# Kernel tuning notes

Hardware: AMD Instinct MI355X
Metric: run time of the kernel (lower is better)

## Reference

```python
import jax, jax.numpy as jnp
import numpy as np

D_MODEL = 1024
NUM_HEADS = 16
D_K = D_MODEL // NUM_HEADS
BATCH = 4
SEQ = 2048


def setup_inputs() -> dict:
    key = jax.random.key(0)
    ks = jax.random.split(key, 12)
    s = 0.02
    inp = {
        "Q": jax.random.normal(ks[0], (BATCH, SEQ, D_MODEL), jnp.float32),
        "K": jax.random.normal(ks[1], (BATCH, SEQ, D_MODEL), jnp.float32),
        "V": jax.random.normal(ks[2], (BATCH, SEQ, D_MODEL), jnp.float32),
        "mask": jnp.tril(jnp.ones((SEQ, SEQ), jnp.int32)),  # causal: 0 = masked
        "Wq": jax.random.normal(ks[3], (D_MODEL, D_MODEL), jnp.float32) * s,
        "bq": jax.random.normal(ks[4], (D_MODEL,), jnp.float32) * s,
        "Wk": jax.random.normal(ks[5], (D_MODEL, D_MODEL), jnp.float32) * s,
        "bk": jax.random.normal(ks[6], (D_MODEL,), jnp.float32) * s,
        "Wv": jax.random.normal(ks[7], (D_MODEL, D_MODEL), jnp.float32) * s,
        "bv": jax.random.normal(ks[8], (D_MODEL,), jnp.float32) * s,
        "Wo": jax.random.normal(ks[9], (D_MODEL, D_MODEL), jnp.float32) * s,
        "bo": jax.random.normal(ks[10], (D_MODEL,), jnp.float32) * s,
    }
    return inp


def _split_heads(x):
    # (b, s, d_model) -> (b, h, s, d_k)
    b, s, _ = x.shape
    return x.reshape(b, s, NUM_HEADS, D_K).transpose(0, 2, 1, 3)


def reference(Q, K, V, mask, Wq, bq, Wk, bk, Wv, bv, Wo, bo):
    # Linear projections (torch Linear: x @ W^T + b)
    q = _split_heads(Q @ Wq.T + bq)  # (b, h, s, dk)
    k = _split_heads(K @ Wk.T + bk)
    v = _split_heads(V @ Wv.T + bv)
    scale = 1.0 / jnp.sqrt(jnp.asarray(D_K, q.dtype))
    scores = jnp.einsum("bhqd,bhkd->bhqk", q, k) * scale  # (b, h, s, s)
    scores = jnp.where(mask == 0, jnp.asarray(-jnp.inf, scores.dtype), scores)
    attn = jax.nn.softmax(scores, axis=-1)
    out = jnp.einsum("bhqk,bhkd->bhqd", attn, v)  # (b, h, s, dk)
    b, h, s, dk = out.shape
    out = out.transpose(0, 2, 1, 3).reshape(b, s, h * dk)  # combine heads
    return out @ Wo.T + bo
```

## Files before the change

### kernel.cpp

```cpp
#include <hip/hip_runtime.h>


typedef _Float16 f16;
typedef _Float16 f16x8 __attribute__((ext_vector_type(8)));
typedef _Float16 f16x4 __attribute__((ext_vector_type(4)));
typedef float floatx4 __attribute__((ext_vector_type(4)));

#define SEQ 2048
#define DM 1024
#define NH 16
#define DK 64
#define MR 8192

__device__ __forceinline__ void gl_lds16(const void* g, void* lds) {
    __builtin_amdgcn_global_load_lds(
        (const __attribute__((address_space(1))) unsigned int*)g,
        (__attribute__((address_space(3))) unsigned int*)lds,
        16, 0, 0);
}

struct ConvArgs {
    const float* s[7];
    f16* d[7];
};

__global__ __launch_bounds__(256) void convk(ConvArgs a) {
    int bx = blockIdx.x;
    int t, base;
    if (bx < 3 * 8192) { t = bx / 8192; base = bx - t * 8192; }
    else { int r = bx - 3 * 8192; t = 3 + r / 1024; base = r - (t - 3) * 1024; }
    int i = base * 256 + threadIdx.x;
    float4 v = ((const float4*)a.s[t])[i];
    f16x4 o;
    o.x = (f16)v.x; o.y = (f16)v.y; o.z = (f16)v.z; o.w = (f16)v.w;
    ((f16x4*)a.d[t])[i] = o;
}

template <int MODE>
__device__ __forceinline__ void gemm_body(
    const f16* __restrict__ A, const f16* __restrict__ W,
    const float* __restrict__ bias, void* __restrict__ outp,
    int m0, int n0, f16* As, f16* Bs)
{
    const int tid = threadIdx.x;
    const int wave = tid >> 6, lane = tid & 63;
    const int quad = lane >> 4, ln = lane & 15;
    const int wr = wave >> 1, wc = wave & 1;

    floatx4 acc[4][4] = {};

    for (int kt = 0; kt < 16; ++kt) {
        const int k0 = kt * 64;
#pragma unroll
        for (int s = 0; s < 4; ++s) {
            int c = s * 256 + tid;
            int row = c >> 3, lc = (c & 7) ^ (row & 7);
            gl_lds16(A + (size_t)(m0 + row) * 1024 + k0 + lc * 8,
                     (char*)As + (s * 256 + wave * 64) * 16);
        }
#pragma unroll
        for (int s = 0; s < 4; ++s) {
            int c = s * 256 + tid;
            int row = c >> 3, lc = (c & 7) ^ (row & 7);
            gl_lds16(W + (size_t)(n0 + row) * 1024 + k0 + lc * 8,
                     (char*)Bs + (s * 256 + wave * 64) * 16);
        }
        __syncthreads();
#pragma unroll
        for (int kk = 0; kk < 64; kk += 32) {
            const int cb = kk >> 3;
            f16x8 af[4], bf[4];
#pragma unroll
            for (int i = 0; i < 4; ++i) {
                int row = wr * 64 + i * 16 + ln;
                af[i] = *(const f16x8*)&As[row * 64 + (((cb + quad) ^ (ln & 7)) << 3)];
            }
#pragma unroll
            for (int j = 0; j < 4; ++j) {
                int row = wc * 64 + j * 16 + ln;
                bf[j] = *(const f16x8*)&Bs[row * 64 + (((cb + quad) ^ (ln & 7)) << 3)];
            }
#pragma unroll
            for (int i = 0; i < 4; ++i)
#pragma unroll
                for (int j = 0; j < 4; ++j)
                    acc[i][j] = __builtin_amdgcn_mfma_f32_16x16x32_f16(
                        af[i], bf[j], acc[i][j], 0, 0, 0);
        }
        __syncthreads();
    }

#pragma unroll
    for (int i = 0; i < 4; ++i) {
#pragma unroll
        for (int j = 0; j < 4; ++j) {
            int col = n0 + wc * 64 + j * 16 + ln;
            float bc = bias[col];
            int rowb = m0 + wr * 64 + i * 16 + quad * 4;
#pragma unroll
            for (int r = 0; r < 4; ++r) {
                float v = acc[i][j][r] + bc;
                int rm = rowb + r;
                if (MODE == 2) {
                    ((float*)outp)[(size_t)rm * 1024 + col] = v;
                } else {
                    int bb = rm >> 11, ss = rm & 2047;
                    int hh = col >> 6, dd = col & 63;
                    f16* o = (f16*)outp;
                    if (MODE == 0)
                        o[(((size_t)(bb * 16 + hh)) * 2048 + ss) * 64 + dd] = (f16)v;
                    else
                        o[(((size_t)(bb * 16 + hh)) * 64 + dd) * 2048 + ss] = (f16)v;
                }
            }
        }
    }
}

struct G3Args {
    const f16* A[3]; const f16* W[3]; const float* b[3]; f16* o[3];
};

__global__ __launch_bounds__(256, 2) void gemm_qkv(G3Args g) {
    __shared__ alignas(16) f16 As[128 * 64];
    __shared__ alignas(16) f16 Bs[128 * 64];
    const int z = blockIdx.z;
    const int m0 = blockIdx.x * 128, n0 = blockIdx.y * 128;
    if (z < 2)
        gemm_body<0>(g.A[z], g.W[z], g.b[z], g.o[z], m0, n0, As, Bs);
    else
        gemm_body<1>(g.A[2], g.W[2], g.b[2], g.o[2], m0, n0, As, Bs);
}

__global__ __launch_bounds__(256, 2) void gemm_out(
    const f16* __restrict__ A, const f16* __restrict__ W,
    const float* __restrict__ bias, float* __restrict__ outp)
{
    __shared__ alignas(16) f16 As[128 * 64];
    __shared__ alignas(16) f16 Bs[128 * 64];
    gemm_body<2>(A, W, bias, outp, blockIdx.x * 128, blockIdx.y * 128, As, Bs);
}

__global__ __launch_bounds__(256, 2) void attn_kernel(
    const f16* __restrict__ Qp, const f16* __restrict__ Kp,
    const f16* __restrict__ Vt, f16* __restrict__ Op)
{
    __shared__ alignas(16) f16 ks[128 * 64];
    __shared__ alignas(16) f16 vs[64 * 128];
    __shared__ alignas(16) f16 ps[128 * 128];

    const int tid = threadIdx.x;
    const int wave = tid >> 6, lane = tid & 63;
    const int quad = lane >> 4, ln = lane & 15;
    const int bh = blockIdx.x;
    const f16* qb = Qp + (size_t)bh * SEQ * DK;
    const f16* kb = Kp + (size_t)bh * SEQ * DK;
    const f16* vb = Vt + (size_t)bh * DK * SEQ;
    const int b = bh >> 4, h = bh & 15;

    f16* pslot = ps + wave * 4096;

    f16x8 ones;
#pragma unroll
    for (int e = 0; e < 8; ++e) ones[e] = (f16)1.0f;

    for (int half = 0; half < 2; ++half) {
        const int jt = half ? (15 - blockIdx.y) : blockIdx.y;
        const int q0 = jt * 128;

#pragma unroll
        for (int s = 0; s < 4; ++s) {
            int c = s * 256 + tid;
            int row = c >> 3, lc = (c & 7) ^ (row & 7);
            gl_lds16(qb + (size_t)(q0 + row) * 64 + lc * 8,
                     (char*)ps + (s * 256 + wave * 64) * 16);
        }
        __syncthreads();
        f16x8 aq[2][2];
#pragma unroll
        for (int mt = 0; mt < 2; ++mt)
#pragma unroll
            for (int kk = 0; kk < 2; ++kk) {
                int row = wave * 32 + mt * 16 + ln;
                f16x8 v = *(const f16x8*)&ps[row * 64 + (((kk * 4 + quad) ^ (ln & 7)) << 3)];
#pragma unroll
                for (int e = 0; e < 8; ++e) v[e] = v[e] * (f16)0.125f;
                aq[mt][kk] = v;
            }

        floatx4 oacc[2][4] = {};
        floatx4 lacc[2] = {};

        const int nk = jt + 1;
        for (int kt = 0; kt < nk; ++kt) {
            const int k0 = kt * 128;
#pragma unroll
            for (int s = 0; s < 4; ++s) {
                int c = s * 256 + tid;
                int row = c >> 3, lc = (c & 7) ^ (row & 7);
                gl_lds16(kb + (size_t)(k0 + row) * 64 + lc * 8,
                         (char*)ks + (s * 256 + wave * 64) * 16);
            }
#pragma unroll
            for (int s = 0; s < 4; ++s) {
                int c = s * 256 + tid;
                int row = c >> 4, lc = (c & 15) ^ (row & 15);
                gl_lds16(vb + (size_t)row * SEQ + k0 + lc * 8,
                         (char*)vs + (s * 256 + wave * 64) * 16);
            }
            __syncthreads();

            floatx4 sacc[2][8] = {};
#pragma unroll
            for (int kk = 0; kk < 2; ++kk) {
                const int pc = ((kk * 4 + quad) ^ (ln & 7)) << 3;
#pragma unroll
                for (int nt = 0; nt < 8; ++nt) {
                    f16x8 bk = *(const f16x8*)&ks[(nt * 16 + ln) * 64 + pc];
#pragma unroll
                    for (int mt = 0; mt < 2; ++mt)
                        sacc[mt][nt] = __builtin_amdgcn_mfma_f32_16x16x32_f16(
                            aq[mt][kk], bk, sacc[mt][nt], 0, 0, 0);
                }
            }

            const bool diag = (k0 == q0);
#pragma unroll
            for (int mt = 0; mt < 2; ++mt) {
                const int rowb = q0 + wave * 32 + mt * 16 + quad * 4;
#pragma unroll
                for (int nt = 0; nt < 8; ++nt) {
                    const int lch = nt * 2 + (ln >> 3);
                    const int off = ln & 7;
                    const int colv = k0 + nt * 16 + ln;
#pragma unroll
                    for (int r = 0; r < 4; ++r) {
                        float t = sacc[mt][nt][r];
                        if (diag && colv > rowb + r) t = -1e30f;
                        float p = __expf(t);
                        int rp = mt * 16 + quad * 4 + r;
                        pslot[rp * 128 + ((lch ^ (rp & 15)) << 3) + off] = (f16)p;
                    }
                }
            }

#pragma unroll
            for (int kk4 = 0; kk4 < 4; ++kk4) {
                f16x8 ap[2];
#pragma unroll
                for (int mt = 0; mt < 2; ++mt) {
                    int rp = mt * 16 + ln;
                    ap[mt] = *(const f16x8*)&pslot[rp * 128 + (((kk4 * 4 + quad) ^ ln) << 3)];
                    lacc[mt] = __builtin_amdgcn_mfma_f32_16x16x32_f16(
                        ap[mt], ones, lacc[mt], 0, 0, 0);
                }
#pragma unroll
                for (int nt2 = 0; nt2 < 4; ++nt2) {
                    int row = nt2 * 16 + ln;
                    f16x8 bv = *(const f16x8*)&vs[row * 128 + (((kk4 * 4 + quad) ^ ln) << 3)];
#pragma unroll
                    for (int mt = 0; mt < 2; ++mt)
                        oacc[mt][nt2] = __builtin_amdgcn_mfma_f32_16x16x32_f16(
                            ap[mt], bv, oacc[mt][nt2], 0, 0, 0);
                }
            }
            __syncthreads();
        }

#pragma unroll
        for (int mt = 0; mt < 2; ++mt) {
            int rowb = q0 + wave * 32 + mt * 16 + quad * 4;
            float inv[4];
#pragma unroll
            for (int r = 0; r < 4; ++r) inv[r] = 1.0f / lacc[mt][r];
#pragma unroll
            for (int nt2 = 0; nt2 < 4; ++nt2) {
                int col = h * 64 + nt2 * 16 + ln;
#pragma unroll
                for (int r = 0; r < 4; ++r) {
                    float v = oacc[mt][nt2][r] * inv[r];
                    Op[((size_t)b * SEQ + rowb + r) * DM + col] = (f16)v;
                }
            }
        }
    }
}

extern "C" void kernel_launch(void* const* d_in, const int* in_sizes, int n_in,
                              void* d_out, int out_size, void* d_ws, size_t ws_size,
                              hipStream_t stream) {
    const float* Q  = (const float*)d_in[0];
    const float* K  = (const float*)d_in[1];
    const float* V  = (const float*)d_in[2];
    const float* Wq = (const float*)d_in[4];
    const float* bq = (const float*)d_in[5];
    const float* Wk = (const float*)d_in[6];
    const float* bk = (const float*)d_in[7];
    const float* Wv = (const float*)d_in[8];
    const float* bv = (const float*)d_in[9];
    const float* Wo = (const float*)d_in[10];
    const float* bo = (const float*)d_in[11];

    char* ws = (char*)d_ws;
    f16* Xq  = (f16*)(ws);
    f16* Xk  = Xq + (size_t)MR * DM;
    f16* Xv  = Xk + (size_t)MR * DM;
    f16* Wqb = Xv + (size_t)MR * DM;
    f16* Wkb = Wqb + (size_t)DM * DM;
    f16* Wvb = Wkb + (size_t)DM * DM;
    f16* Wob = Wvb + (size_t)DM * DM;
    f16* qp  = Wob + (size_t)DM * DM;
    f16* kp  = qp + (size_t)MR * DM;
    f16* vtp = kp + (size_t)MR * DM;

    ConvArgs ca;
    ca.s[0] = Q;  ca.d[0] = Xq;
    ca.s[1] = K;  ca.d[1] = Xk;
    ca.s[2] = V;  ca.d[2] = Xv;
    ca.s[3] = Wq; ca.d[3] = Wqb;
    ca.s[4] = Wk; ca.d[4] = Wkb;
    ca.s[5] = Wv; ca.d[5] = Wvb;
    ca.s[6] = Wo; ca.d[6] = Wob;
    convk<<<3 * 8192 + 4 * 1024, 256, 0, stream>>>(ca);

    G3Args g;
    g.A[0] = Xq; g.W[0] = Wqb; g.b[0] = bq; g.o[0] = qp;
    g.A[1] = Xk; g.W[1] = Wkb; g.b[1] = bk; g.o[1] = kp;
    g.A[2] = Xv; g.W[2] = Wvb; g.b[2] = bv; g.o[2] = vtp;
    gemm_qkv<<<dim3(64, 8, 3), 256, 0, stream>>>(g);

    attn_kernel<<<dim3(64, 8), 256, 0, stream>>>(qp, kp, vtp, Xq);

    gemm_out<<<dim3(64, 8), 256, 0, stream>>>(Xq, Wob, bo, (float*)d_out);
}
```

Baseline: 308.6 us.

## Fuse fp32-to-fp16 conversion into GEMM tile loads and specialise diagonal attention tile

Removes the separate conversion kernel: the projection GEMMs load fp32 activations and weights directly into LDS via global_load_lds and convert to fp16 when building MFMA fragments. The output GEMM reads fp32 weights the same way. The attention inner loop is factored into a templated iteration so only the final diagonal tile evaluates the causal mask, and the P buffer swizzle is altered. This trades an extra full read and write pass over the inputs for doubled LDS footprint and traffic and extra conversion work inside the GEMM inner loops.

Measured after the change: 349.7 us. 13.3% more time.

```diff
diff --git a/kernel.cpp b/kernel.cpp
--- a/kernel.cpp
+++ b/kernel.cpp
@@ -3,7 +3,7 @@
 
 typedef _Float16 f16;
 typedef _Float16 f16x8 __attribute__((ext_vector_type(8)));
-typedef _Float16 f16x4 __attribute__((ext_vector_type(4)));
+typedef __fp16 h16x2 __attribute__((ext_vector_type(2)));
 typedef float floatx4 __attribute__((ext_vector_type(4)));
 
 #define SEQ 2048
@@ -19,28 +19,26 @@
         16, 0, 0);
 }
 
-struct ConvArgs {
-    const float* s[7];
-    f16* d[7];
-};
-
-__global__ __launch_bounds__(256) void convk(ConvArgs a) {
-    int bx = blockIdx.x;
-    int t, base;
-    if (bx < 3 * 8192) { t = bx / 8192; base = bx - t * 8192; }
-    else { int r = bx - 3 * 8192; t = 3 + r / 1024; base = r - (t - 3) * 1024; }
-    int i = base * 256 + threadIdx.x;
-    float4 v = ((const float4*)a.s[t])[i];
-    f16x4 o;
-    o.x = (f16)v.x; o.y = (f16)v.y; o.z = (f16)v.z; o.w = (f16)v.w;
-    ((f16x4*)a.d[t])[i] = o;
-}
-
-template <int MODE>
+__device__ __forceinline__ f16x8 frag_from_f32(const float* Ls, int row, int c0) {
+    const int p0 = (c0 ^ (row & 15));
+    const int p1 = ((c0 + 1) ^ (row & 15));
+    float4 lo = *(const float4*)&Ls[row * 64 + p0 * 4];
+    float4 hi = *(const float4*)&Ls[row * 64 + p1 * 4];
+    h16x2 h0 = __builtin_amdgcn_cvt_pkrtz(lo.x, lo.y);
+    h16x2 h1 = __builtin_amdgcn_cvt_pkrtz(lo.z, lo.w);
+    h16x2 h2 = __builtin_amdgcn_cvt_pkrtz(hi.x, hi.y);
+    h16x2 h3 = __builtin_amdgcn_cvt_pkrtz(hi.z, hi.w);
+    f16x8 o;
+    o[0] = (f16)h0[0]; o[1] = (f16)h0[1]; o[2] = (f16)h1[0]; o[3] = (f16)h1[1];
+    o[4] = (f16)h2[0]; o[5] = (f16)h2[1]; o[6] = (f16)h3[0]; o[7] = (f16)h3[1];
+    return o;
+}
+
+template <int MODE, bool AF32>
 __device__ __forceinline__ void gemm_body(
-    const f16* __restrict__ A, const f16* __restrict__ W,
+    const void* __restrict__ A, const float* __restrict__ W,
     const float* __restrict__ bias, void* __restrict__ outp,
-    int m0, int n0, f16* As, f16* Bs)
+    int m0, int n0, void* AsMem, float* Bsf)
 {
     const int tid = threadIdx.x;
     const int wave = tid >> 6, lane = tid & 63;
@@ -51,35 +49,49 @@
 
     for (int kt = 0; kt < 16; ++kt) {
         const int k0 = kt * 64;
-#pragma unroll
-        for (int s = 0; s < 4; ++s) {
+        if constexpr (AF32) {
+#pragma unroll
+            for (int s = 0; s < 8; ++s) {
+                int c = s * 256 + tid;
+                int row = c >> 4, lc = (c & 15) ^ (row & 15);
+                gl_lds16((const float*)A + (size_t)(m0 + row) * 1024 + k0 + lc * 4,
+                         (char*)AsMem + (s * 256 + wave * 64) * 16);
+            }
+        } else {
+#pragma unroll
+            for (int s = 0; s < 4; ++s) {
+                int c = s * 256 + tid;
+                int row = c >> 3, lc = (c & 7) ^ (row & 7);
+                gl_lds16((const f16*)A + (size_t)(m0 + row) * 1024 + k0 + lc * 8,
+                         (char*)AsMem + (s * 256 + wave * 64) * 16);
+            }
+        }
+#pragma unroll
+        for (int s = 0; s < 8; ++s) {
             int c = s * 256 + tid;
-            int row = c >> 3, lc = (c & 7) ^ (row & 7);
-            gl_lds16(A + (size_t)(m0 + row) * 1024 + k0 + lc * 8,
-                     (char*)As + (s * 256 + wave * 64) * 16);
-        }
-#pragma unroll
-        for (int s = 0; s < 4; ++s) {
-            int c = s * 256 + tid;
-            int row = c >> 3, lc = (c & 7) ^ (row & 7);
-            gl_lds16(W + (size_t)(n0 + row) * 1024 + k0 + lc * 8,
-                     (char*)Bs + (s * 256 + wave * 64) * 16);
+            int row = c >> 4, lc = (c & 15) ^ (row & 15);
+            gl_lds16(W + (size_t)(n0 + row) * 1024 + k0 + lc * 4,
+                     (char*)Bsf + (s * 256 + wave * 64) * 16);
         }
         __syncthreads();
 #pragma unroll
         for (int kk = 0; kk < 64; kk += 32) {
-            const int cb = kk >> 3;
+            const int c0 = (kk >> 2) + quad * 2;
             f16x8 af[4], bf[4];
 #pragma unroll
             for (int i = 0; i < 4; ++i) {
                 int row = wr * 64 + i * 16 + ln;
-                af[i] = *(const f16x8*)&As[row * 64 + (((cb + quad) ^ (ln & 7)) << 3)];
-            }
-#pragma unroll
-            for (int j = 0; j < 4; ++j) {
-                int row = wc * 64 + j * 16 + ln;
-                bf[j] = *(const f16x8*)&Bs[row * 64 + (((cb + quad) ^ (ln & 7)) << 3)];
-            }
+                if constexpr (AF32) {
+                    af[i] = frag_from_f32((const float*)AsMem, row, c0);
+                } else {
+                    const int cb = kk >> 3;
+                    af[i] = *(const f16x8*)&((const f16*)AsMem)
+                        [row * 64 + (((cb + quad) ^ (ln & 7)) << 3)];
+                }
+            }
+#pragma unroll
+            for (int j = 0; j < 4; ++j)
+                bf[j] = frag_from_f32(Bsf, wc * 64 + j * 16 + ln, c0);
 #pragma unroll
             for (int i = 0; i < 4; ++i)
 #pragma unroll
@@ -118,27 +130,110 @@
 }
 
 struct G3Args {
-    const f16* A[3]; const f16* W[3]; const float* b[3]; f16* o[3];
+    const float* A[3]; const float* W[3]; const float* b[3]; f16* o[3];
 };
 
 __global__ __launch_bounds__(256, 2) void gemm_qkv(G3Args g) {
-    __shared__ alignas(16) f16 As[128 * 64];
-    __shared__ alignas(16) f16 Bs[128 * 64];
+    __shared__ alignas(16) float Asf[128 * 64];
+    __shared__ alignas(16) float Bsf[128 * 64];
     const int z = blockIdx.z;
     const int m0 = blockIdx.x * 128, n0 = blockIdx.y * 128;
     if (z < 2)
-        gemm_body<0>(g.A[z], g.W[z], g.b[z], g.o[z], m0, n0, As, Bs);
+        gemm_body<0, true>(g.A[z], g.W[z], g.b[z], g.o[z], m0, n0, Asf, Bsf);
     else
-        gemm_body<1>(g.A[2], g.W[2], g.b[2], g.o[2], m0, n0, As, Bs);
+        gemm_body<1, true>(g.A[2], g.W[2], g.b[2], g.o[2], m0, n0, Asf, Bsf);
 }
 
 __global__ __launch_bounds__(256, 2) void gemm_out(
-    const f16* __restrict__ A, const f16* __restrict__ W,
+    const f16* __restrict__ A, const float* __restrict__ W,
     const float* __restrict__ bias, float* __restrict__ outp)
 {
-    __shared__ alignas(16) f16 As[128 * 64];
-    __shared__ alignas(16) f16 Bs[128 * 64];
-    gemm_body<2>(A, W, bias, outp, blockIdx.x * 128, blockIdx.y * 128, As, Bs);
+    __shared__ alignas(16) f16 Ash[128 * 64];
+    __shared__ alignas(16) float Bsf[128 * 64];
+    gemm_body<2, false>(A, W, bias, outp, blockIdx.x * 128, blockIdx.y * 128,
+                        Ash, Bsf);
+}
+
+template <bool DIAG>
+__device__ __forceinline__ void attn_iter(
+    const f16* kb, const f16* vb, int k0, int q0,
+    f16* ks, f16* vs, f16* pslot,
+    int tid, int wave, int quad, int ln,
+    const f16x8 (&aq)[2][2], const f16x8& ones,
+    floatx4 (&oacc)[2][4], floatx4 (&lacc)[2])
+{
+#pragma unroll
+    for (int s = 0; s < 4; ++s) {
+        int c = s * 256 + tid;
+        int row = c >> 3, lc = (c & 7) ^ (row & 7);
+        gl_lds16(kb + (size_t)(k0 + row) * 64 + lc * 8,
+                 (char*)ks + (s * 256 + wave * 64) * 16);
+    }
+#pragma unroll
+    for (int s = 0; s < 4; ++s) {
+        int c = s * 256 + tid;
+        int row = c >> 4, lc = (c & 15) ^ (row & 15);
+        gl_lds16(vb + (size_t)row * SEQ + k0 + lc * 8,
+                 (char*)vs + (s * 256 + wave * 64) * 16);
+    }
+    __syncthreads();
+
+    floatx4 sacc[2][8] = {};
+#pragma unroll
+    for (int kk = 0; kk < 2; ++kk) {
+        const int pc = ((kk * 4 + quad) ^ (ln & 7)) << 3;
+#pragma unroll
+        for (int nt = 0; nt < 8; ++nt) {
+            f16x8 bk = *(const f16x8*)&ks[(nt * 16 + ln) * 64 + pc];
+#pragma unroll
+            for (int mt = 0; mt < 2; ++mt)
+                sacc[mt][nt] = __builtin_amdgcn_mfma_f32_16x16x32_f16(
+                    aq[mt][kk], bk, sacc[mt][nt], 0, 0, 0);
+        }
+    }
+
+#pragma unroll
+    for (int mt = 0; mt < 2; ++mt) {
+        const int rowb = q0 + wave * 32 + mt * 16 + quad * 4;
+#pragma unroll
+        for (int nt = 0; nt < 8; ++nt) {
+            const int lch = nt * 2 + (ln >> 3);
+            const int off = ln & 7;
+            const int colv = k0 + nt * 16 + ln;
+#pragma unroll
+            for (int r = 0; r < 4; ++r) {
+                float t = sacc[mt][nt][r];
+                if (DIAG && colv > rowb + r) t = -1e30f;
+                float p = __expf(t);
+                const int rp = mt * 16 + quad * 4 + r;
+                const int sw = (rp & 15) ^ (((rp >> 3) & 1) << 1);
+                pslot[rp * 128 + ((lch ^ sw) << 3) + off] = (f16)p;
+            }
+        }
+    }
+
+#pragma unroll
+    for (int kk4 = 0; kk4 < 4; ++kk4) {
+        f16x8 ap[2];
+#pragma unroll
+        for (int mt = 0; mt < 2; ++mt) {
+            const int rp = mt * 16 + ln;
+            const int sw = (rp & 15) ^ (((rp >> 3) & 1) << 1);
+            ap[mt] = *(const f16x8*)&pslot[rp * 128 + (((kk4 * 4 + quad) ^ sw) << 3)];
+            lacc[mt] = __builtin_amdgcn_mfma_f32_16x16x32_f16(
+                ap[mt], ones, lacc[mt], 0, 0, 0);
+        }
+#pragma unroll
+        for (int nt2 = 0; nt2 < 4; ++nt2) {
+            int row = nt2 * 16 + ln;
+            f16x8 bv = *(const f16x8*)&vs[row * 128 + (((kk4 * 4 + quad) ^ ln) << 3)];
+#pragma unroll
+            for (int mt = 0; mt < 2; ++mt)
+                oacc[mt][nt2] = __builtin_amdgcn_mfma_f32_16x16x32_f16(
+                    ap[mt], bv, oacc[mt][nt2], 0, 0, 0);
+        }
+    }
+    __syncthreads();
 }
 
 __global__ __launch_bounds__(256, 2) void attn_kernel(
@@ -192,80 +287,11 @@
         floatx4 lacc[2] = {};
 
         const int nk = jt + 1;
-        for (int kt = 0; kt < nk; ++kt) {
-            const int k0 = kt * 128;
-#pragma unroll
-            for (int s = 0; s < 4; ++s) {
-                int c = s * 256 + tid;
-                int row = c >> 3, lc = (c & 7) ^ (row & 7);
-                gl_lds16(kb + (size_t)(k0 + row) * 64 + lc * 8,
-                         (char*)ks + (s * 256 + wave * 64) * 16);
-            }
-#pragma unroll
-            for (int s = 0; s < 4; ++s) {
-                int c = s * 256 + tid;
-                int row = c >> 4, lc = (c & 15) ^ (row & 15);
-                gl_lds16(vb + (size_t)row * SEQ + k0 + lc * 8,
-                         (char*)vs + (s * 256 + wave * 64) * 16);
-            }
-            __syncthreads();
-
-            floatx4 sacc[2][8] = {};
-#pragma unroll
-            for (int kk = 0; kk < 2; ++kk) {
-                const int pc = ((kk * 4 + quad) ^ (ln & 7)) << 3;
-#pragma unroll
-                for (int nt = 0; nt < 8; ++nt) {
-                    f16x8 bk = *(const f16x8*)&ks[(nt * 16 + ln) * 64 + pc];
-#pragma unroll
-                    for (int mt = 0; mt < 2; ++mt)
-                        sacc[mt][nt] = __builtin_amdgcn_mfma_f32_16x16x32_f16(
-                            aq[mt][kk], bk, sacc[mt][nt], 0, 0, 0);
-                }
-            }
-
-            const bool diag = (k0 == q0);
-#pragma unroll
-            for (int mt = 0; mt < 2; ++mt) {
-                const int rowb = q0 + wave * 32 + mt * 16 + quad * 4;
-#pragma unroll
-                for (int nt = 0; nt < 8; ++nt) {
-                    const int lch = nt * 2 + (ln >> 3);
-                    const int off = ln & 7;
-                    const int colv = k0 + nt * 16 + ln;
-#pragma unroll
-                    for (int r = 0; r < 4; ++r) {
-                        float t = sacc[mt][nt][r];
-                        if (diag && colv > rowb + r) t = -1e30f;
-                        float p = __expf(t);
-                        int rp = mt * 16 + quad * 4 + r;
-                        pslot[rp * 128 + ((lch ^ (rp & 15)) << 3) + off] = (f16)p;
-                    }
-                }
-            }
-
-#pragma unroll
-            for (int kk4 = 0; kk4 < 4; ++kk4) {
-                f16x8 ap[2];
-#pragma unroll
-                for (int mt = 0; mt < 2; ++mt) {
-                    int rp = mt * 16 + ln;
-                    ap[mt] = *(const f16x8*)&pslot[rp * 128 + (((kk4 * 4 + quad) ^ ln) << 3)];
-                    lacc[mt] = __builtin_amdgcn_mfma_f32_16x16x32_f16(
-                        ap[mt], ones, lacc[mt], 0, 0, 0);
-                }
-#pragma unroll
-                for (int nt2 = 0; nt2 < 4; ++nt2) {
-                    int row = nt2 * 16 + ln;
-                    f16x8 bv = *(const f16x8*)&vs[row * 128 + (((kk4 * 4 + quad) ^ ln) << 3)];
-#pragma unroll
-                    for (int mt = 0; mt < 2; ++mt)
-                        oacc[mt][nt2] = __builtin_amdgcn_mfma_f32_16x16x32_f16(
-                            ap[mt], bv, oacc[mt][nt2], 0, 0, 0);
-                }
-            }
-            __syncthreads();
-        }
+        for (int kt = 0; kt < nk - 1; ++kt)
+            attn_iter<false>(kb, vb, kt * 128, q0, ks, vs, pslot,
+                             tid, wave, quad, ln, aq, ones, oacc, lacc);
+        attn_iter<true>(kb, vb, (nk - 1) * 128, q0, ks, vs, pslot,
+                        tid, wave, quad, ln, aq, ones, oacc, lacc);
 
 #pragma unroll
         for (int mt = 0; mt < 2; ++mt) {
@@ -302,34 +328,18 @@
     const float* bo = (const float*)d_in[11];
 
     char* ws = (char*)d_ws;
-    f16* Xq  = (f16*)(ws);
-    f16* Xk  = Xq + (size_t)MR * DM;
-    f16* Xv  = Xk + (size_t)MR * DM;
-    f16* Wqb = Xv + (size_t)MR * DM;
-    f16* Wkb = Wqb + (size_t)DM * DM;
-    f16* Wvb = Wkb + (size_t)DM * DM;
-    f16* Wob = Wvb + (size_t)DM * DM;
-    f16* qp  = Wob + (size_t)DM * DM;
+    f16* qp  = (f16*)ws;
     f16* kp  = qp + (size_t)MR * DM;
     f16* vtp = kp + (size_t)MR * DM;
-
-    ConvArgs ca;
-    ca.s[0] = Q;  ca.d[0] = Xq;
-    ca.s[1] = K;  ca.d[1] = Xk;
-    ca.s[2] = V;  ca.d[2] = Xv;
-    ca.s[3] = Wq; ca.d[3] = Wqb;
-    ca.s[4] = Wk; ca.d[4] = Wkb;
-    ca.s[5] = Wv; ca.d[5] = Wvb;
-    ca.s[6] = Wo; ca.d[6] = Wob;
-    convk<<<3 * 8192 + 4 * 1024, 256, 0, stream>>>(ca);
+    f16* ao  = vtp + (size_t)MR * DM;
 
     G3Args g;
-    g.A[0] = Xq; g.W[0] = Wqb; g.b[0] = bq; g.o[0] = qp;
-    g.A[1] = Xk; g.W[1] = Wkb; g.b[1] = bk; g.o[1] = kp;
-    g.A[2] = Xv; g.W[2] = Wvb; g.b[2] = bv; g.o[2] = vtp;
+    g.A[0] = Q; g.W[0] = Wq; g.b[0] = bq; g.o[0] = qp;
+    g.A[1] = K; g.W[1] = Wk; g.b[1] = bk; g.o[1] = kp;
+    g.A[2] = V; g.W[2] = Wv; g.b[2] = bv; g.o[2] = vtp;
     gemm_qkv<<<dim3(64, 8, 3), 256, 0, stream>>>(g);
 
-    attn_kernel<<<dim3(64, 8), 256, 0, stream>>>(qp, kp, vtp, Xq);
-
-    gemm_out<<<dim3(64, 8), 256, 0, stream>>>(Xq, Wob, bo, (float*)d_out);
-}
+    attn_kernel<<<dim3(64, 8), 256, 0, stream>>>(qp, kp, vtp, ao);
+
+    gemm_out<<<dim3(64, 8), 256, 0, stream>>>(ao, Wo, bo, (float*)d_out);
+}
```
